# Optimization experiments

Hardware: AMD Instinct MI355X
Metric: run time of the kernel (lower is better)

## Reference

```python
import jax, jax.numpy as jnp
import numpy as np

V, E, H, B, P, Q = 100000, 300, 256, 64, 400, 50
NEG = -1e7


def _gru_param(k, s=0.08):
    k1, k2, k3, k4 = jax.random.split(k, 4)
    return (jax.random.normal(k1, (2, 3 * H, E)) * s,
            jax.random.normal(k2, (2, 3 * H, H)) * s,
            jax.random.normal(k3, (2, 3 * H)) * s,
            jax.random.normal(k4, (2, 3 * H)) * s)


def setup_inputs() -> dict:
    key = jax.random.key(0)
    ks = jax.random.split(key, 10)
    emb = (jax.random.normal(ks[0], (V, E)) * 0.1).at[0].set(0.0)  # padding_idx=0 row zeroed
    passage = jax.random.randint(ks[1], (B, P), 1, V)
    question = jax.random.randint(ks[2], (B, Q), 1, V)
    # variable lengths, padding (token 0) at the tail like pack_padded_sequence assumes
    p_len = 200 + (jnp.arange(B) * 7) % (P - 200)
    q_len = 20 + (jnp.arange(B) * 3) % (Q - 20)
    passage = jnp.where(jnp.arange(P)[None, :] < p_len[:, None], passage, 0)
    question = jnp.where(jnp.arange(Q)[None, :] < q_len[:, None], question, 0)
    pW_ih, pW_hh, pb_ih, pb_hh = _gru_param(ks[3])
    qW_ih, qW_hh, qb_ih, qb_hh = _gru_param(ks[4])
    start_w = jax.random.normal(ks[5], (6 * H,)) * 0.05
    start_b = jax.random.normal(ks[6], ()) * 0.05
    end_w = jax.random.normal(ks[7], (6 * H,)) * 0.05
    end_b = jax.random.normal(ks[8], ()) * 0.05
    return dict(passage=passage, question=question, emb=emb,
                pW_ih=pW_ih, pW_hh=pW_hh, pb_ih=pb_ih, pb_hh=pb_hh,
                qW_ih=qW_ih, qW_hh=qW_hh, qb_ih=qb_ih, qb_hh=qb_hh,
                start_w=start_w, start_b=start_b, end_w=end_w, end_b=end_b)


def bi_gru(x, mask, Wih, Whh, bih, bhh):
    """Bidirectional GRU with packed-sequence-equivalent masking.
    x: (B,T,E), mask: (B,T) float. Returns (B,T,2H). Padded outputs are 0,
    and the backward pass starts at the true last token (mask freezes state)."""
    m = mask[..., None]                                          # (B,T,1)
    xproj = jnp.einsum('bte,dhe->dbth', x, Wih) + bih[:, None, None, :]  # (2,B,T,3H)

    def run(xp, mm, Whh_d, bhh_d):
        def step(h, inp):
            xt, mt = inp                                         # (B,3H),(B,1)
            hp = h @ Whh_d.T + bhh_d
            r = jax.nn.sigmoid(xt[:, :H] + hp[:, :H])
            z = jax.nn.sigmoid(xt[:, H:2 * H] + hp[:, H:2 * H])
            n = jnp.tanh(xt[:, 2 * H:] + r * hp[:, 2 * H:])
            h_new = (1 - z) * n + z * h
            h_new = mt * h_new + (1 - mt) * h
            return h_new, h_new * mt
        h0 = jnp.zeros((xp.shape[0], H), xp.dtype)
        _, out = jax.lax.scan(step, h0, (xp.transpose(1, 0, 2), mm.transpose(1, 0, 2)))
        return out.transpose(1, 0, 2)                            # (B,T,H)

    fwd = run(xproj[0], m, Whh[0], bhh[0])
    bwd = run(xproj[1][:, ::-1], m[:, ::-1], Whh[1], bhh[1])[:, ::-1]
    return jnp.concatenate([fwd, bwd], axis=-1)


def reference(passage, question, emb,
              pW_ih, pW_hh, pb_ih, pb_hh,
              qW_ih, qW_hh, qb_ih, qb_hh,
              start_w, start_b, end_w, end_b):
    p_mask = (passage != 0).astype(jnp.float32)                  # (B,P)
    q_mask = (question != 0).astype(jnp.float32)                 # (B,Q)
    Hp = bi_gru(emb[passage], p_mask, pW_ih, pW_hh, pb_ih, pb_hh)  # (B,P,2H)
    Hq = bi_gru(emb[question], q_mask, qW_ih, qW_hh, qb_ih, qb_hh)  # (B,Q,2H)

    # Trilinear attention: decompose Linear over the cat([p, q, p*q]) terms
    w1, w2, w3 = start_w[:2 * H], start_w[2 * H:4 * H], start_w[4 * H:]
    scores = (Hp @ w1)[:, :, None] + (Hq @ w2)[:, None, :] \
        + jnp.einsum('bpd,bqd->bpq', Hp * w3, Hq) + start_b      # (B,P,Q)

    # allennlp masked_softmax: softmax(vector*mask) * mask, renormalized
    a = jax.nn.softmax(scores * q_mask[:, None, :], axis=-1) * q_mask[:, None, :]
    a = a / (a.sum(axis=-1, keepdims=True) + 1e-13)

    wavg = jnp.einsum('bpq,bqd->bpd', a, Hq)                     # (B,P,2H)
    combined = jnp.concatenate([Hp, wavg, Hp * wavg], axis=-1)   # (B,P,6H)

    start_logits = jnp.where(p_mask > 0, combined @ start_w + start_b, NEG)
    end_logits = jnp.where(p_mask > 0, combined @ end_w + end_b, NEG)
    log_mask = jnp.log(p_mask + 1e-45)
    softmax_start = jax.nn.log_softmax(start_logits + log_mask, axis=-1)
    softmax_end = jax.nn.log_softmax(end_logits + log_mask, axis=-1)
    return start_logits, end_logits, softmax_start, softmax_end
```

## Files before the change

kernel.cpp:

```cpp
#include <hip/hip_runtime.h>
#include <math.h>

constexpr int Bb = 64;
constexpr int Pp = 400;
constexpr int Qq = 50;
constexpr int Ee = 300;
constexpr int Hh = 256;
constexpr int H3 = 768;
constexpr int Dd = 512;

#define NEGC (-10000000.0f)
#define LOGTINY (-103.278929903f)

typedef _Float16 h2 __attribute__((ext_vector_type(2)));
typedef _Float16 f16x8 __attribute__((ext_vector_type(8)));
typedef float f32x4 __attribute__((ext_vector_type(4)));

__device__ __forceinline__ float allred(float v){
  #pragma unroll
  for (int off = 1; off < 64; off <<= 1) v += __shfl_xor(v, off);
  return v;
}
__device__ __forceinline__ float allmax(float v){
  #pragma unroll
  for (int off = 1; off < 64; off <<= 1) v = fmaxf(v, __shfl_xor(v, off));
  return v;
}
__device__ __forceinline__ float sigm(float x){ return 1.f / (1.f + expf(-x)); }

__device__ __forceinline__ float dot2f(unsigned a, unsigned b, float c){
#if __has_builtin(__builtin_amdgcn_fdot2)
  return __builtin_amdgcn_fdot2(__builtin_bit_cast(h2, a), __builtin_bit_cast(h2, b), c, false);
#else
  float r = c;
  asm("v_dot2_f32_f16 %0, %1, %2, %0" : "+v"(r) : "v"(a), "v"(b));
  return r;
#endif
}

#define U4C(v,c) ((c)==0?(v).x:((c)==1?(v).y:((c)==2?(v).z:(v).w)))

__global__ __launch_bounds__(256) void prep_w16(const float* __restrict__ pW,
                                                const float* __restrict__ qW,
                                                unsigned* __restrict__ w16){
  int idx = blockIdx.x * 256 + threadIdx.x;
  if (idx >= 2 * 2 * 3 * 16 * 512 * 4) return;
  int c = idx & 3;
  int t = (idx >> 2) & 511;
  int q = (idx >> 11) & 15;
  int gg = idx >> 15;
  int gate = gg % 3, gd = gg / 3;
  int d = gd & 1, g = gd >> 1;
  int j = t & 255, half = t >> 8;
  int p = half * 64 + q * 4 + c;
  int row = gate * 256 + j;
  const float* W = g ? qW : pW;
  const float* src = W + ((size_t)d * H3 + row) * Hh + 2 * p;
  _Float16 a = (_Float16)src[0], b = (_Float16)src[1];
  unsigned short ua, ub;
  __builtin_memcpy(&ua, &a, 2); __builtin_memcpy(&ub, &b, 2);
  unsigned val = (unsigned)ua | ((unsigned)ub << 16);

  size_t u4idx;
  if (q < 4)       u4idx = ((size_t)gg * 4 + q) * 512 + t;
  else if (q < 10) u4idx = 24576 + ((size_t)gg * 6 + (q - 4)) * 512 + t;
  else             u4idx = 61440 + ((size_t)gg * 6 + (q - 10)) * 512 + t;
  w16[u4idx * 4 + c] = val;
}

__global__ __launch_bounds__(512) void xproj_mfma(const int* __restrict__ tok,
                                                  const float* __restrict__ emb,
                                                  const float* __restrict__ Wih,
                                                  const float* __restrict__ bih,
                                                  _Float16* __restrict__ xp, int T){
  __shared__ __align__(16) _Float16 As[128][72];
  __shared__ __align__(16) _Float16 Bs[128][72];
  int tid = threadIdx.x;
  int m0 = blockIdx.y * 128;
  int nt = blockIdx.x;
  int d = nt / 6, h0 = (nt % 6) * 128;
  int wid = tid >> 6, lane = tid & 63;
  int wr = wid >> 2, wc = wid & 3;

  int srow = tid >> 2;
  int scol = (tid & 3) * 16;
  const float* aRow = emb + (size_t)tok[m0 + srow] * Ee;
  const float* bRow = Wih + ((size_t)d * H3 + h0 + srow) * Ee;

  f32x4 acc[4][2] = {};

  for (int k0 = 0; k0 < 320; k0 += 64){
    #pragma unroll
    for (int half = 0; half < 2; ++half){
      int k = k0 + scol + half * 8;
      float4 va0, va1, vb0, vb1;
      if (k + 8 <= Ee){
        va0 = *(const float4*)(aRow + k); va1 = *(const float4*)(aRow + k + 4);
        vb0 = *(const float4*)(bRow + k); vb1 = *(const float4*)(bRow + k + 4);
      } else if (k + 4 <= Ee){
        va0 = *(const float4*)(aRow + k); va1 = make_float4(0.f, 0.f, 0.f, 0.f);
        vb0 = *(const float4*)(bRow + k); vb1 = make_float4(0.f, 0.f, 0.f, 0.f);
      } else {
        va0 = va1 = vb0 = vb1 = make_float4(0.f, 0.f, 0.f, 0.f);
      }
      f16x8 a8 = { (_Float16)va0.x, (_Float16)va0.y, (_Float16)va0.z, (_Float16)va0.w,
                   (_Float16)va1.x, (_Float16)va1.y, (_Float16)va1.z, (_Float16)va1.w };
      f16x8 b8 = { (_Float16)vb0.x, (_Float16)vb0.y, (_Float16)vb0.z, (_Float16)vb0.w,
                   (_Float16)vb1.x, (_Float16)vb1.y, (_Float16)vb1.z, (_Float16)vb1.w };
      *(f16x8*)&As[srow][scol + half * 8] = a8;
      *(f16x8*)&Bs[srow][scol + half * 8] = b8;
    }
    __syncthreads();
    #pragma unroll
    for (int kc = 0; kc < 2; ++kc){
      int kb = kc * 32 + (lane >> 4) * 8;
      f16x8 af[4], bf[2];
      #pragma unroll
      for (int i = 0; i < 4; ++i) af[i] = *(const f16x8*)&As[wr * 64 + i * 16 + (lane & 15)][kb];
      #pragma unroll
      for (int jn = 0; jn < 2; ++jn) bf[jn] = *(const f16x8*)&Bs[wc * 32 + jn * 16 + (lane & 15)][kb];
      #pragma unroll
      for (int i = 0; i < 4; ++i)
        #pragma unroll
        for (int jn = 0; jn < 2; ++jn)
          acc[i][jn] = __builtin_amdgcn_mfma_f32_16x16x32_f16(af[i], bf[jn], acc[i][jn], 0, 0, 0);
    }
    __syncthreads();
  }

  #pragma unroll
  for (int jn = 0; jn < 2; ++jn){
    int h = h0 + wc * 32 + jn * 16 + (lane & 15);
    float bv = bih[d * H3 + h];
    #pragma unroll
    for (int i = 0; i < 4; ++i){
      #pragma unroll
      for (int r = 0; r < 4; ++r){
        int m = m0 + wr * 64 + i * 16 + (lane >> 4) * 4 + r;
        int bI = m / T, tI = m - bI * T;
        xp[(((size_t)d * Bb + bI) * T + tI) * H3 + h] = (_Float16)(acc[i][jn][r] + bv);
      }
    }
  }
}

__global__ __launch_bounds__(512)
void gru_kernel(const int* __restrict__ ptok,
                const int* __restrict__ qtok,
                const _Float16* __restrict__ xpp,
                const _Float16* __restrict__ xpq,
                const unsigned* __restrict__ w16,
                const float* __restrict__ pbhh,
                const float* __restrict__ qbhh,
                float* __restrict__ Hp,
                float* __restrict__ Hq){
  int wg = blockIdx.x;
  bool isp = wg < 128;
  int lw = isp ? wg : wg - 128;
  int d = lw & 1, b = lw >> 1;
  int T = isp ? Pp : Qq;
  const int* tok = (isp ? ptok : qtok) + b * T;
  const _Float16* xrow = (isp ? xpp : xpq) + ((size_t)d * Bb + b) * T * H3;
  int gd = (isp ? 0 : 2) + d;
  const float* bhh = (isp ? pbhh : qbhh) + d * H3;
  float* Hout = (isp ? Hp : Hq) + (size_t)b * T * Dd + d * Hh;

  __shared__ __align__(16) uint4 ldsW[18 * 512];
  __shared__ unsigned hbuf[2][128];
  __shared__ float pa[Hh], pb[Hh], pn[Hh];

  int t = threadIdx.x;
  int j = t & 255, half = t >> 8, lane = t & 63;

  const uint4* wR = (const uint4*)w16 + (size_t)(gd * 3) * 4 * 512;
  unsigned wr0[16], wr1[16], wr2[16];
  #pragma unroll
  for (int q = 0; q < 4; ++q){
    uint4 v0 = wR[(0 * 4 + q) * 512 + t];
    uint4 v1 = wR[(1 * 4 + q) * 512 + t];
    uint4 v2 = wR[(2 * 4 + q) * 512 + t];
    wr0[4 * q + 0] = v0.x; wr0[4 * q + 1] = v0.y; wr0[4 * q + 2] = v0.z; wr0[4 * q + 3] = v0.w;
    wr1[4 * q + 0] = v1.x; wr1[4 * q + 1] = v1.y; wr1[4 * q + 2] = v1.z; wr1[4 * q + 3] = v1.w;
    wr2[4 * q + 0] = v2.x; wr2[4 * q + 1] = v2.y; wr2[4 * q + 2] = v2.z; wr2[4 * q + 3] = v2.w;
  }
  #pragma unroll
  for (int i = 0; i < 16; ++i){
    asm volatile("" : "+v"(wr0[i]));
    asm volatile("" : "+v"(wr1[i]));
    asm volatile("" : "+v"(wr2[i]));
  }
  const uint4* wL = (const uint4*)w16 + 24576 + (size_t)(gd * 3) * 6 * 512;
  #pragma unroll
  for (int u = 0; u < 18; ++u) ldsW[u * 512 + t] = wL[u * 512 + t];
  const uint4* wS = (const uint4*)w16 + 61440 + (size_t)(gd * 3) * 6 * 512;

  float bh0 = bhh[j], bh1 = bhh[Hh + j], bh2 = bhh[2 * Hh + j];
  float h_old = 0.f;
  if (t < 128) hbuf[1][t] = 0u;
  __syncthreads();

  int t0 = d ? (T - 1) : 0;
  float pre0 = 0.f, pre1 = 0.f, pre2 = 0.f;
  if (half == 0){
    pre0 = (float)xrow[(size_t)t0 * H3 + j];
    pre1 = (float)xrow[(size_t)t0 * H3 + Hh + j];
    pre2 = (float)xrow[(size_t)t0 * H3 + 2 * Hh + j];
  }

  for (int s = 0; s < T; ++s){
    int tt = d ? (T - 1 - s) : s;
    unsigned vh = hbuf[(s + 1) & 1][half * 64 + lane];
    float a0 = 0.f, a1 = 0.f, a2 = 0.f;

    uint4 sA0 = wS[0 * 512 + t], sA1 = wS[1 * 512 + t], sA2 = wS[2 * 512 + t],
          sA3 = wS[3 * 512 + t], sA4 = wS[4 * 512 + t], sA5 = wS[5 * 512 + t];

    #pragma unroll
    for (int q = 0; q < 4; ++q)
      #pragma unroll
      for (int c = 0; c < 4; ++c){
        unsigned hv = (unsigned)__builtin_amdgcn_readlane((int)vh, q * 4 + c);
        a0 = dot2f(wr0[4 * q + c], hv, a0);
        a1 = dot2f(wr1[4 * q + c], hv, a1);
        a2 = dot2f(wr2[4 * q + c], hv, a2);
      }

    #pragma unroll
    for (int qb = 0; qb < 6; ++qb){
      uint4 l0 = ldsW[(0 * 6 + qb) * 512 + t];
      uint4 l1 = ldsW[(1 * 6 + qb) * 512 + t];
      uint4 l2 = ldsW[(2 * 6 + qb) * 512 + t];
      #pragma unroll
      for (int c = 0; c < 4; ++c){
        unsigned hv = (unsigned)__builtin_amdgcn_readlane((int)vh, 16 + qb * 4 + c);
        a0 = dot2f(U4C(l0, c), hv, a0);
        a1 = dot2f(U4C(l1, c), hv, a1);
        a2 = dot2f(U4C(l2, c), hv, a2);
      }
    }

    #define CONS(v, qi, ACC) { _Pragma("unroll") \
      for (int c = 0; c < 4; ++c){ \
        unsigned hv = (unsigned)__builtin_amdgcn_readlane((int)vh, 40 + (qi) * 4 + c); \
        ACC = dot2f(U4C(v, c), hv, ACC); } }
    uint4 sB0 = wS[6 * 512 + t],  sB1 = wS[7 * 512 + t],  sB2 = wS[8 * 512 + t],
          sB3 = wS[9 * 512 + t],  sB4 = wS[10 * 512 + t], sB5 = wS[11 * 512 + t];
    CONS(sA0, 0, a0) CONS(sA1, 1, a0) CONS(sA2, 2, a0)
    CONS(sA3, 3, a0) CONS(sA4, 4, a0) CONS(sA5, 5, a0)
    uint4 sC0 = wS[12 * 512 + t], sC1 = wS[13 * 512 + t], sC2 = wS[14 * 512 + t],
          sC3 = wS[15 * 512 + t], sC4 = wS[16 * 512 + t], sC5 = wS[17 * 512 + t];
    CONS(sB0, 0, a1) CONS(sB1, 1, a1) CONS(sB2, 2, a1)
    CONS(sB3, 3, a1) CONS(sB4, 4, a1) CONS(sB5, 5, a1)
    CONS(sC0, 0, a2) CONS(sC1, 1, a2) CONS(sC2, 2, a2)
    CONS(sC3, 3, a2) CONS(sC4, 4, a2) CONS(sC5, 5, a2)
    #undef CONS

    if (half == 1){ pa[j] = a0; pb[j] = a1; pn[j] = a2; }
    __syncthreads();
    if (half == 0){
      float xt0 = pre0, xt1 = pre1, xt2 = pre2;
      if (s + 1 < T){
        int tn = d ? (T - 2 - s) : (s + 1);
        pre0 = (float)xrow[(size_t)tn * H3 + j];
        pre1 = (float)xrow[(size_t)tn * H3 + Hh + j];
        pre2 = (float)xrow[(size_t)tn * H3 + 2 * Hh + j];
      }
      float g0 = a0 + pa[j] + bh0;
      float g1 = a1 + pb[j] + bh1;
      float g2 = a2 + pn[j] + bh2;
      float r = sigm(xt0 + g0);
      float z = sigm(xt1 + g1);
      float n = tanhf(xt2 + r * g2);
      float hnew = (1.f - z) * n + z * h_old;
      float m = (tok[tt] != 0) ? 1.f : 0.f;
      float hm = m * hnew + (1.f - m) * h_old;
      h_old = hm;
      ((_Float16*)hbuf[s & 1])[j] = (_Float16)hm;
      Hout[(size_t)tt * Dd + j] = hm * m;
    }
    __syncthreads();
  }
}

__global__ __launch_bounds__(512) void attn_kernel(const float* __restrict__ Hp,
                                                   const float* __restrict__ Hq,
                                                   const int* __restrict__ ptok,
                                                   const int* __restrict__ qtok,
                                                   const float* __restrict__ start_w,
                                                   const float* __restrict__ sbp,
                                                   const float* __restrict__ end_w,
                                                   const float* __restrict__ ebp,
                                                   float* __restrict__ out){
  extern __shared__ __align__(16) float lds[];
  float* hqs = lds;
  float* s2s = hqs + Qq * Dd;
  float* qms = s2s + 64;
  float* scw = qms + 64;
  float* aw  = scw + 512;

  int b = blockIdx.y, pc = blockIdx.x;
  int tid = threadIdx.x, wid = tid >> 6, lane = tid & 63;
  float sb = sbp[0], eb = ebp[0];

  float w1r[8], w2r[8], w3r[8], e1r[8], e2r[8], e3r[8];
  #pragma unroll
  for (int i = 0; i < 8; ++i){
    int c = lane * 8 + i;
    w1r[i] = start_w[c]; w2r[i] = start_w[Dd + c]; w3r[i] = start_w[2 * Dd + c];
    e1r[i] = end_w[c];   e2r[i] = end_w[Dd + c];   e3r[i] = end_w[2 * Dd + c];
  }
  for (int idx = tid; idx < Qq * Dd; idx += 512) hqs[idx] = Hq[(size_t)b * Qq * Dd + idx];
  __syncthreads();

  for (int q = wid; q < Qq; q += 8){
    float part = 0.f;
    const float* hq = hqs + q * Dd + lane * 8;
    #pragma unroll
    for (int i = 0; i < 8; ++i) part += hq[i] * w2r[i];
    part = allred(part);
    if (lane == 0){
      s2s[q] = part;
      qms[q] = (qtok[b * Qq + q] != 0) ? 1.f : 0.f;
    }
  }
  __syncthreads();

  for (int p = pc * 100 + wid; p < pc * 100 + 100; p += 8){
    const float* hprow = Hp + ((size_t)b * Pp + p) * Dd + lane * 8;
    float4 hv0 = *(const float4*)hprow;
    float4 hv1 = *(const float4*)(hprow + 4);
    float hpc[8] = {hv0.x, hv0.y, hv0.z, hv0.w, hv1.x, hv1.y, hv1.z, hv1.w};
    float hw3[8], he3[8];
    float s1 = 0.f, ed = 0.f;
    #pragma unroll
    for (int i = 0; i < 8; ++i){
      hw3[i] = hpc[i] * w3r[i];
      he3[i] = hpc[i] * e3r[i];
      s1 += hpc[i] * w1r[i];
      ed += hpc[i] * e1r[i];
    }
    #pragma unroll
    for (int off = 1; off < 64; off <<= 1){
      s1 += __shfl_xor(s1, off);
      ed += __shfl_xor(ed, off);
    }
    for (int q = 0; q < Qq; ++q){
      const float4* hq4 = (const float4*)(hqs + q * Dd + lane * 8);
      float4 a0 = hq4[0], a1 = hq4[1];
      float dot = hw3[0] * a0.x + hw3[1] * a0.y + hw3[2] * a0.z + hw3[3] * a0.w
                + hw3[4] * a1.x + hw3[5] * a1.y + hw3[6] * a1.z + hw3[7] * a1.w;
      dot = allred(dot);
      if (lane == 0) scw[wid * 64 + q] = (s1 + s2s[q] + dot + sb) * qms[q];
    }
    float v = (lane < Qq) ? scw[wid * 64 + lane] : -1e30f;
    float M = allmax(v);
    float ev = (lane < Qq) ? expf(v - M) : 0.f;
    float S = allred(ev);
    float am = (lane < Qq) ? (ev / S) * qms[lane] : 0.f;
    float Sm = allred(am);
    float af = am / (Sm + 1e-13f);
    if (lane < Qq) aw[wid * 64 + lane] = af;
    float wv[8] = {0.f, 0.f, 0.f, 0.f, 0.f, 0.f, 0.f, 0.f};
    for (int q = 0; q < Qq; ++q){
      float aq = aw[wid * 64 + q];
      const float4* hq4 = (const float4*)(hqs + q * Dd + lane * 8);
      float4 a0 = hq4[0], a1 = hq4[1];
      wv[0] += aq * a0.x; wv[1] += aq * a0.y; wv[2] += aq * a0.z; wv[3] += aq * a0.w;
      wv[4] += aq * a1.x; wv[5] += aq * a1.y; wv[6] += aq * a1.z; wv[7] += aq * a1.w;
    }
    float acc2 = 0.f, acc3 = 0.f, acc4 = 0.f, acc5 = 0.f;
    #pragma unroll
    for (int i = 0; i < 8; ++i){
      acc2 += wv[i] * w2r[i];
      acc3 += hw3[i] * wv[i];
      acc4 += wv[i] * e2r[i];
      acc5 += he3[i] * wv[i];
    }
    #pragma unroll
    for (int off = 1; off < 64; off <<= 1){
      acc2 += __shfl_xor(acc2, off);
      acc3 += __shfl_xor(acc3, off);
      acc4 += __shfl_xor(acc4, off);
      acc5 += __shfl_xor(acc5, off);
    }
    if (lane == 0){
      bool pm = (ptok[b * Pp + p] != 0);
      out[(size_t)b * Pp + p]                   = pm ? (s1 + acc2 + acc3 + sb) : NEGC;
      out[(size_t)Bb * Pp + (size_t)b * Pp + p] = pm ? (ed + acc4 + acc5 + eb) : NEGC;
    }
  }
}

__global__ __launch_bounds__(512) void lsm_kernel(const int* __restrict__ ptok,
                                                  float* __restrict__ out){
  int b = blockIdx.x >> 1, sel = blockIdx.x & 1;
  const float* lg = out + (size_t)sel * Bb * Pp + (size_t)b * Pp;
  float* o = out + (size_t)(2 + sel) * Bb * Pp + (size_t)b * Pp;
  int tid = threadIdx.x;
  __shared__ float red1[8];
  __shared__ float red2[8];
  float x = -1e30f;
  if (tid < Pp) x = lg[tid] + ((ptok[b * Pp + tid] != 0) ? 0.f : LOGTINY);
  float m = allmax(x);
  if ((tid & 63) == 0) red1[tid >> 6] = m;
  __syncthreads();
  float M = red1[0];
  #pragma unroll
  for (int i = 1; i < 8; ++i) M = fmaxf(M, red1[i]);
  float e = (tid < Pp) ? expf(x - M) : 0.f;
  float s = allred(e);
  if ((tid & 63) == 0) red2[tid >> 6] = s;
  __syncthreads();
  float S = 0.f;
  #pragma unroll
  for (int i = 0; i < 8; ++i) S += red2[i];
  if (tid < Pp) o[tid] = (x - M) - logf(S);
}

extern "C" void kernel_launch(void* const* d_in, const int* in_sizes, int n_in,
                              void* d_out, int out_size, void* d_ws, size_t ws_size,
                              hipStream_t stream){
  const int*   passage  = (const int*)d_in[0];
  const int*   question = (const int*)d_in[1];
  const float* emb      = (const float*)d_in[2];
  const float* pW_ih    = (const float*)d_in[3];
  const float* pW_hh    = (const float*)d_in[4];
  const float* pb_ih    = (const float*)d_in[5];
  const float* pb_hh    = (const float*)d_in[6];
  const float* qW_ih    = (const float*)d_in[7];
  const float* qW_hh    = (const float*)d_in[8];
  const float* qb_ih    = (const float*)d_in[9];
  const float* qb_hh    = (const float*)d_in[10];
  const float* start_w  = (const float*)d_in[11];
  const float* start_b  = (const float*)d_in[12];
  const float* end_w    = (const float*)d_in[13];
  const float* end_b    = (const float*)d_in[14];
  float* out = (float*)d_out;

  float*     ws  = (float*)d_ws;
  unsigned*  w16 = (unsigned*)ws;
  _Float16*  xpp = (_Float16*)(ws + 393216);
  _Float16*  xpq = (_Float16*)(ws + 20054016);
  float*     Hp  = ws + 22511616;
  float*     Hq  = ws + 35618816;

  hipLaunchKernelGGL(prep_w16, dim3(1536), dim3(256), 0, stream, pW_hh, qW_hh, w16);
  hipLaunchKernelGGL(xproj_mfma, dim3(12, 200), dim3(512), 0, stream,
                     passage, emb, pW_ih, pb_ih, xpp, Pp);
  hipLaunchKernelGGL(xproj_mfma, dim3(12, 25), dim3(512), 0, stream,
                     question, emb, qW_ih, qb_ih, xpq, Qq);
  hipLaunchKernelGGL(gru_kernel, dim3(256), dim3(512), 0, stream,
                     passage, question, xpp, xpq, w16, pb_hh, qb_hh, Hp, Hq);
  size_t attn_lds = (size_t)(Qq * Dd + 64 + 64 + 512 + 512) * sizeof(float);
  hipLaunchKernelGGL(attn_kernel, dim3(4, 64), dim3(512), attn_lds, stream,
                     Hp, Hq, passage, question, start_w, start_b, end_w, end_b, out);
  hipLaunchKernelGGL(lsm_kernel, dim3(128), dim3(512), 0, stream, passage, out);
}
```

Baseline: 972.8 us.

## Pre-convert embedding table and input weights to fp16 padded layout for xproj

Adds two pre-pass kernels that convert the full embedding table and the GRU input weights to fp16, padded to 320 columns, so the xproj MFMA kernel can load f16x8 directly with no per-tile conversion or bounds checks. It also moves the wS register loads in the GRU step earlier to overlap them with compute. The cost is that the entire 100k×300 embedding table is converted on every call, which reads 120MB and writes 64MB, even though only the gathered rows (about 28k tokens) are needed.

Result: no change. 964.3 us (-0.9%).

```diff
diff --git a/kernel.cpp b/kernel.cpp
--- a/kernel.cpp
+++ b/kernel.cpp
@@ -39,6 +39,36 @@
 }
 
 #define U4C(v,c) ((c)==0?(v).x:((c)==1?(v).y:((c)==2?(v).z:(v).w)))
+
+__global__ __launch_bounds__(256) void prep_emb16(const float* __restrict__ emb,
+                                                  _Float16* __restrict__ emb16){
+  size_t idx = (size_t)blockIdx.x * 256 + threadIdx.x;
+  if (idx >= (size_t)100000 * 160) return;
+  int col2 = (int)(idx % 160);
+  size_t row = idx / 160;
+  int c = col2 * 2;
+  float2 v = make_float2(0.f, 0.f);
+  if (c < Ee) v = *(const float2*)(emb + row * Ee + c);
+  h2 o = { (_Float16)v.x, (_Float16)v.y };
+  *(h2*)(emb16 + row * 320 + c) = o;
+}
+
+__global__ __launch_bounds__(256) void prep_wih16(const float* __restrict__ pW,
+                                                  const float* __restrict__ qW,
+                                                  _Float16* __restrict__ wih16){
+  int idx = blockIdx.x * 256 + threadIdx.x;
+  if (idx >= 2 * 2 * 768 * 160) return;
+  int col2 = idx % 160;
+  int r = idx / 160;
+  int g = r / 1536;
+  int dh = r % 1536;
+  int c = col2 * 2;
+  const float* W = g ? qW : pW;
+  float2 v = make_float2(0.f, 0.f);
+  if (c < Ee) v = *(const float2*)(W + (size_t)dh * Ee + c);
+  h2 o = { (_Float16)v.x, (_Float16)v.y };
+  *(h2*)(wih16 + (size_t)r * 320 + c) = o;
+}
 
 __global__ __launch_bounds__(256) void prep_w16(const float* __restrict__ pW,
                                                 const float* __restrict__ qW,
@@ -69,12 +99,12 @@
 }
 
 __global__ __launch_bounds__(512) void xproj_mfma(const int* __restrict__ tok,
-                                                  const float* __restrict__ emb,
-                                                  const float* __restrict__ Wih,
+                                                  const _Float16* __restrict__ emb16,
+                                                  const _Float16* __restrict__ wih16,
                                                   const float* __restrict__ bih,
                                                   _Float16* __restrict__ xp, int T){
-  __shared__ __align__(16) _Float16 As[128][72];
-  __shared__ __align__(16) _Float16 Bs[128][72];
+  __shared__ __align__(16) _Float16 Af[128][72];
+  __shared__ __align__(16) _Float16 Bf[128][72];
   int tid = threadIdx.x;
   int m0 = blockIdx.y * 128;
   int nt = blockIdx.x;
@@ -82,43 +112,30 @@
   int wid = tid >> 6, lane = tid & 63;
   int wr = wid >> 2, wc = wid & 3;
 
-  int srow = tid >> 2;
-  int scol = (tid & 3) * 16;
-  const float* aRow = emb + (size_t)tok[m0 + srow] * Ee;
-  const float* bRow = Wih + ((size_t)d * H3 + h0 + srow) * Ee;
+  int r0 = tid >> 3;
+  int r1 = (tid + 512) >> 3;
+  int cc = (tid & 7) * 8;
+  const _Float16* eA0 = emb16 + (size_t)tok[m0 + r0] * 320;
+  const _Float16* eA1 = emb16 + (size_t)tok[m0 + r1] * 320;
+  const _Float16* wB0 = wih16 + ((size_t)d * H3 + h0 + r0) * 320;
+  const _Float16* wB1 = wih16 + ((size_t)d * H3 + h0 + r1) * 320;
 
   f32x4 acc[4][2] = {};
 
   for (int k0 = 0; k0 < 320; k0 += 64){
-    #pragma unroll
-    for (int half = 0; half < 2; ++half){
-      int k = k0 + scol + half * 8;
-      float4 va0, va1, vb0, vb1;
-      if (k + 8 <= Ee){
-        va0 = *(const float4*)(aRow + k); va1 = *(const float4*)(aRow + k + 4);
-        vb0 = *(const float4*)(bRow + k); vb1 = *(const float4*)(bRow + k + 4);
-      } else if (k + 4 <= Ee){
-        va0 = *(const float4*)(aRow + k); va1 = make_float4(0.f, 0.f, 0.f, 0.f);
-        vb0 = *(const float4*)(bRow + k); vb1 = make_float4(0.f, 0.f, 0.f, 0.f);
-      } else {
-        va0 = va1 = vb0 = vb1 = make_float4(0.f, 0.f, 0.f, 0.f);
-      }
-      f16x8 a8 = { (_Float16)va0.x, (_Float16)va0.y, (_Float16)va0.z, (_Float16)va0.w,
-                   (_Float16)va1.x, (_Float16)va1.y, (_Float16)va1.z, (_Float16)va1.w };
-      f16x8 b8 = { (_Float16)vb0.x, (_Float16)vb0.y, (_Float16)vb0.z, (_Float16)vb0.w,
-                   (_Float16)vb1.x, (_Float16)vb1.y, (_Float16)vb1.z, (_Float16)vb1.w };
-      *(f16x8*)&As[srow][scol + half * 8] = a8;
-      *(f16x8*)&Bs[srow][scol + half * 8] = b8;
-    }
+    *(f16x8*)&Af[r0][cc] = *(const f16x8*)(eA0 + k0 + cc);
+    *(f16x8*)&Af[r1][cc] = *(const f16x8*)(eA1 + k0 + cc);
+    *(f16x8*)&Bf[r0][cc] = *(const f16x8*)(wB0 + k0 + cc);
+    *(f16x8*)&Bf[r1][cc] = *(const f16x8*)(wB1 + k0 + cc);
     __syncthreads();
     #pragma unroll
     for (int kc = 0; kc < 2; ++kc){
       int kb = kc * 32 + (lane >> 4) * 8;
       f16x8 af[4], bf[2];
       #pragma unroll
-      for (int i = 0; i < 4; ++i) af[i] = *(const f16x8*)&As[wr * 64 + i * 16 + (lane & 15)][kb];
-      #pragma unroll
-      for (int jn = 0; jn < 2; ++jn) bf[jn] = *(const f16x8*)&Bs[wc * 32 + jn * 16 + (lane & 15)][kb];
+      for (int i = 0; i < 4; ++i) af[i] = *(const f16x8*)&Af[wr * 64 + i * 16 + (lane & 15)][kb];
+      #pragma unroll
+      for (int jn = 0; jn < 2; ++jn) bf[jn] = *(const f16x8*)&Bf[wc * 32 + jn * 16 + (lane & 15)][kb];
       #pragma unroll
       for (int i = 0; i < 4; ++i)
         #pragma unroll
@@ -214,6 +231,8 @@
 
     uint4 sA0 = wS[0 * 512 + t], sA1 = wS[1 * 512 + t], sA2 = wS[2 * 512 + t],
           sA3 = wS[3 * 512 + t], sA4 = wS[4 * 512 + t], sA5 = wS[5 * 512 + t];
+    uint4 sB0 = wS[6 * 512 + t],  sB1 = wS[7 * 512 + t],  sB2 = wS[8 * 512 + t],
+          sB3 = wS[9 * 512 + t],  sB4 = wS[10 * 512 + t], sB5 = wS[11 * 512 + t];
 
     #pragma unroll
     for (int q = 0; q < 4; ++q)
@@ -225,6 +244,9 @@
         a2 = dot2f(wr2[4 * q + c], hv, a2);
       }
 
+    uint4 sC0 = wS[12 * 512 + t], sC1 = wS[13 * 512 + t], sC2 = wS[14 * 512 + t],
+          sC3 = wS[15 * 512 + t], sC4 = wS[16 * 512 + t], sC5 = wS[17 * 512 + t];
+
     #pragma unroll
     for (int qb = 0; qb < 6; ++qb){
       uint4 l0 = ldsW[(0 * 6 + qb) * 512 + t];
@@ -243,12 +265,8 @@
       for (int c = 0; c < 4; ++c){ \
         unsigned hv = (unsigned)__builtin_amdgcn_readlane((int)vh, 40 + (qi) * 4 + c); \
         ACC = dot2f(U4C(v, c), hv, ACC); } }
-    uint4 sB0 = wS[6 * 512 + t],  sB1 = wS[7 * 512 + t],  sB2 = wS[8 * 512 + t],
-          sB3 = wS[9 * 512 + t],  sB4 = wS[10 * 512 + t], sB5 = wS[11 * 512 + t];
     CONS(sA0, 0, a0) CONS(sA1, 1, a0) CONS(sA2, 2, a0)
     CONS(sA3, 3, a0) CONS(sA4, 4, a0) CONS(sA5, 5, a0)
-    uint4 sC0 = wS[12 * 512 + t], sC1 = wS[13 * 512 + t], sC2 = wS[14 * 512 + t],
-          sC3 = wS[15 * 512 + t], sC4 = wS[16 * 512 + t], sC5 = wS[17 * 512 + t];
     CONS(sB0, 0, a1) CONS(sB1, 1, a1) CONS(sB2, 2, a1)
     CONS(sB3, 3, a1) CONS(sB4, 4, a1) CONS(sB5, 5, a1)
     CONS(sC0, 0, a2) CONS(sC1, 1, a2) CONS(sC2, 2, a2)
@@ -437,18 +455,22 @@
   const float* end_b    = (const float*)d_in[14];
   float* out = (float*)d_out;
 
-  float*     ws  = (float*)d_ws;
-  unsigned*  w16 = (unsigned*)ws;
-  _Float16*  xpp = (_Float16*)(ws + 393216);
-  _Float16*  xpq = (_Float16*)(ws + 20054016);
-  float*     Hp  = ws + 22511616;
-  float*     Hq  = ws + 35618816;
+  float*     ws    = (float*)d_ws;
+  unsigned*  w16   = (unsigned*)ws;
+  _Float16*  emb16 = (_Float16*)(ws + 393216);
+  _Float16*  wih16 = (_Float16*)(ws + 16393216);
+  _Float16*  xpp   = (_Float16*)(ws + 16884736);
+  _Float16*  xpq   = (_Float16*)(ws + 36545536);
+  float*     Hp    = ws + 39003136;
+  float*     Hq    = ws + 52110336;
 
   hipLaunchKernelGGL(prep_w16, dim3(1536), dim3(256), 0, stream, pW_hh, qW_hh, w16);
+  hipLaunchKernelGGL(prep_emb16, dim3(62500), dim3(256), 0, stream, emb, emb16);
+  hipLaunchKernelGGL(prep_wih16, dim3(1920), dim3(256), 0, stream, pW_ih, qW_ih, wih16);
   hipLaunchKernelGGL(xproj_mfma, dim3(12, 200), dim3(512), 0, stream,
-                     passage, emb, pW_ih, pb_ih, xpp, Pp);
+                     passage, emb16, wih16, pb_ih, xpp, Pp);
   hipLaunchKernelGGL(xproj_mfma, dim3(12, 25), dim3(512), 0, stream,
-                     question, emb, qW_ih, qb_ih, xpq, Qq);
+                     question, emb16, wih16 + (size_t)2 * H3 * 320, qb_ih, xpq, Qq);
   hipLaunchKernelGGL(gru_kernel, dim3(256), dim3(512), 0, stream,
                      passage, question, xpp, xpq, w16, pb_hh, qb_hh, Hp, Hq);
   size_t attn_lds = (size_t)(Qq * Dd + 64 + 64 + 512 + 512) * sizeof(float);
```
